# Performance work log

Measured on AMD Instinct MI355X. Metric: run time of the kernel, lower is better.

## Reference

```python
import jax, jax.numpy as jnp
import numpy as np

N, E, F_IN, DIM, HEADS, L, G, NC = 10000, 160000, 512, 256, 4, 3, 16, 10
HID = HEADS * DIM  # 1024


def gat_layer(x, src, dst, W, a_src, a_dst, b):
    # x: [N, in], W: [in, H*D], a_src/a_dst: [H, D], b: [H*D]
    h = (x @ W).reshape(N, HEADS, DIM)                       # [N,H,D]
    e_src = jnp.einsum('nhd,hd->nh', h, a_src)               # [N,H]
    e_dst = jnp.einsum('nhd,hd->nh', h, a_dst)               # [N,H]
    e = jax.nn.leaky_relu(e_src[src] + e_dst[dst], 0.2)      # [E,H]
    # segment softmax over edges grouped by destination node
    emax = jax.ops.segment_max(e, dst, num_segments=N)       # [N,H]
    ee = jnp.exp(e - emax[dst])
    denom = jax.ops.segment_sum(ee, dst, num_segments=N)     # [N,H]
    alpha = ee / denom[dst]                                  # [E,H]
    msg = h[src] * alpha[:, :, None]                         # [E,H,D]
    out = jax.ops.segment_sum(msg, dst, num_segments=N)      # [N,H,D]
    return out.reshape(N, HID) + b


def setup_inputs() -> dict:
    key = jax.random.key(0)
    ks = jax.random.split(key, 12)
    x = jax.random.normal(ks[0], (N, F_IN), dtype=jnp.float32)
    edge_index = jax.random.randint(ks[1], (2, E), 0, N, dtype=jnp.int32)
    batch = jnp.sort(jax.random.randint(ks[2], (N,), 0, G, dtype=jnp.int32))
    s0 = 1.0 / np.sqrt(F_IN)
    s1 = 1.0 / np.sqrt(HID)
    sd = 1.0 / np.sqrt(DIM)
    W0 = jax.random.normal(ks[3], (F_IN, HID), dtype=jnp.float32) * s0
    W1 = jax.random.normal(ks[4], (HID, HID), dtype=jnp.float32) * s1
    W2 = jax.random.normal(ks[5], (HID, HID), dtype=jnp.float32) * s1
    a_src = jax.random.normal(ks[6], (L, HEADS, DIM), dtype=jnp.float32) * sd
    a_dst = jax.random.normal(ks[7], (L, HEADS, DIM), dtype=jnp.float32) * sd
    bias = jnp.zeros((L, HID), dtype=jnp.float32)
    fc_w = jax.random.normal(ks[8], (HID, NC), dtype=jnp.float32) * s1
    fc_b = jnp.zeros((NC,), dtype=jnp.float32)
    return {"x": x, "edge_index": edge_index, "batch": batch, "W0": W0,
            "W1": W1, "W2": W2, "a_src": a_src, "a_dst": a_dst,
            "bias": bias, "fc_w": fc_w, "fc_b": fc_b}


def reference(x, edge_index, batch, W0, W1, W2, a_src, a_dst, bias, fc_w, fc_b):
    # add self-loops (PyG GATConv default)
    loop = jnp.arange(N, dtype=edge_index.dtype)
    src = jnp.concatenate([edge_index[0], loop])
    dst = jnp.concatenate([edge_index[1], loop])
    Ws = [W0, W1, W2]
    h = x
    for l in range(L):
        h = gat_layer(h, src, dst, Ws[l], a_src[l], a_dst[l], bias[l])
        h = jax.nn.relu(h)  # Dropout(0.5) is identity in eval mode
    # global mean pool over graphs
    sums = jax.ops.segment_sum(h, batch, num_segments=G)            # [G,HID]
    cnts = jax.ops.segment_sum(jnp.ones((N,), h.dtype), batch, num_segments=G)
    pooled = sums / jnp.maximum(cnts, 1.0)[:, None]
    logits = pooled @ fc_w + fc_b
    return jax.nn.log_softmax(logits, axis=-1)
```

## Files before the change

kernel.cpp:

```cpp
#include <hip/hip_runtime.h>
#include <math.h>

#define NNODES 10000
#define HID    1024
#define NHEADS 4
#define NGRAPH 16
#define NCLS   10

typedef __attribute__((ext_vector_type(8))) short bf16x8;
typedef __attribute__((ext_vector_type(8))) ushort u16x8;
typedef __attribute__((ext_vector_type(4))) float f32x4;
typedef __attribute__((ext_vector_type(2))) float f32x2;

__device__ __forceinline__ ushort bf16r(float f) {
    union { float f; unsigned u; } x; x.f = f;
    unsigned r = x.u + 0x7FFFu + ((x.u >> 16) & 1u);
    return (ushort)(r >> 16);
}
__device__ __forceinline__ float bf16f(ushort u) {
    union { unsigned u; float f; } x; x.u = ((unsigned)u) << 16;
    return x.f;
}
__device__ __forceinline__ float leaky(float e) { return e > 0.f ? e : 0.2f * e; }


__global__ void k_hist(const int* __restrict__ dstArr, int* __restrict__ counts,
                       const int* __restrict__ batch, int* __restrict__ gstart,
                       int* __restrict__ gend, int E, int N) {
    int e = blockIdx.x * 256 + threadIdx.x;
    int total = E + N;
    if (e < total) {
        int d = (e < E) ? dstArr[e] : (e - E);
        atomicAdd(&counts[d], 1);
    }
    if (e < N) {
        int g = batch[e];
        if (e == 0 || batch[e - 1] != g) gstart[g] = e;
        if (e == N - 1 || batch[e + 1] != g) gend[g] = e + 1;
    }
}

__global__ __launch_bounds__(1024) void k_scan(const int* __restrict__ counts,
                                               int* __restrict__ row_ptr, int N) {
    __shared__ int lds[1024];
    int t = threadIdx.x;
    const int C = (N + 1023) / 1024;
    int base = t * C;
    int s = 0;
    for (int i = 0; i < C; ++i)
        if (base + i < N) s += counts[base + i];
    lds[t] = s;
    __syncthreads();
    for (int off = 1; off < 1024; off <<= 1) {
        int add = (t >= off) ? lds[t - off] : 0;
        __syncthreads();
        lds[t] += add;
        __syncthreads();
    }
    int run = lds[t] - s;
    for (int i = 0; i < C; ++i) {
        if (base + i < N) {
            row_ptr[base + i] = run;
            run += counts[base + i];
        }
    }
    if (t == 1023) row_ptr[N] = lds[1023];
}

__global__ void k_scatter(const int* __restrict__ srcArr, const int* __restrict__ dstArr,
                          const int* __restrict__ row_ptr, int* __restrict__ fill,
                          int* __restrict__ col, int E) {
    int e = blockIdx.x * 256 + threadIdx.x;
    int total = E + NNODES;
    if (e < total) {
        int s, d;
        if (e < E) { s = srcArr[e]; d = dstArr[e]; }
        else       { s = d = e - E; }
        int pos = row_ptr[d] + atomicAdd(&fill[d], 1);
        col[pos] = s;
    }
}


__global__ void k_f32_to_bf16(const float* __restrict__ in, ushort* __restrict__ out, int n4) {
    int i = blockIdx.x * 256 + threadIdx.x;
    if (i < n4) {
        float4 v = ((const float4*)in)[i];
        ushort4 o;
        o.x = bf16r(v.x); o.y = bf16r(v.y); o.z = bf16r(v.z); o.w = bf16r(v.w);
        ((ushort4*)out)[i] = o;
    }
}

__global__ __launch_bounds__(256) void k_wT3(const float* __restrict__ W0,
                                             const float* __restrict__ W1,
                                             const float* __restrict__ W2,
                                             ushort* __restrict__ w0t,
                                             ushort* __restrict__ w1t,
                                             ushort* __restrict__ w2t) {
    __shared__ ushort tile[32][33];
    int z = blockIdx.z;
    const float* W = (z == 0) ? W0 : (z == 1) ? W1 : W2;
    ushort* Wt     = (z == 0) ? w0t : (z == 1) ? w1t : w2t;
    int K          = (z == 0) ? 512 : HID;
    int bx = blockIdx.x;
    int by = blockIdx.y;
    if (by * 32 >= K) return;
    int tx = threadIdx.x & 31, ty = threadIdx.x >> 5;
#pragma unroll
    for (int i = 0; i < 32; i += 8) {
        int k  = by * 32 + ty + i;
        int nn = bx * 32 + tx;
        tile[ty + i][tx] = bf16r(W[(size_t)k * HID + nn]);
    }
    __syncthreads();
#pragma unroll
    for (int i = 0; i < 32; i += 8) {
        int nn = bx * 32 + ty + i;
        int k  = by * 32 + tx;
        Wt[(size_t)nn * K + k] = tile[tx][ty + i];
    }
}


#define BM 128
#define BN 128
#define BK 64

__global__ __launch_bounds__(256) void k_gemm_bf16(const ushort* __restrict__ A,
                                                   const ushort* __restrict__ Bt,
                                                   ushort* __restrict__ C, int M, int K) {
    __shared__ ushort As[BM * BK];
    __shared__ ushort Bs[BN * BK];
    const int t    = threadIdx.x;
    const int lane = t & 63;
    const int w    = t >> 6;
    const int wr   = w >> 1, wc = w & 1;
    const int bm   = blockIdx.y * BM;
    const int bn   = blockIdx.x * BN;

    f32x4 acc[4][4] = {};

    const int r_  = t >> 3;
    const int cp_ = t & 7;

    const ushort* aSrc[4];
    const ushort* bSrc[4];
#pragma unroll
    for (int i = 0; i < 4; ++i) {
        int r  = i * 32 + r_;
        int c  = cp_ ^ (r & 7);
        int ga = bm + r; if (ga >= M) ga = M - 1;
        aSrc[i] = &A[(size_t)ga * K + c * 8];
        bSrc[i] = &Bt[(size_t)(bn + r) * K + c * 8];
    }

    for (int k0 = 0; k0 < K; k0 += BK) {
        __syncthreads();
#pragma unroll
        for (int i = 0; i < 4; ++i) {
            int fc = i * 256 + t;
            __builtin_amdgcn_global_load_lds(
                (const __attribute__((address_space(1))) unsigned*)(aSrc[i] + k0),
                (__attribute__((address_space(3))) unsigned*)&As[fc * 8], 16, 0, 0);
            __builtin_amdgcn_global_load_lds(
                (const __attribute__((address_space(1))) unsigned*)(bSrc[i] + k0),
                (__attribute__((address_space(3))) unsigned*)&Bs[fc * 8], 16, 0, 0);
        }
        __syncthreads();

#pragma unroll
        for (int s = 0; s < 2; ++s) {
            const int kc = s * 4 + (lane >> 4);
            bf16x8 a[4], b[4];
#pragma unroll
            for (int m = 0; m < 4; ++m) {
                int row = wr * 64 + m * 16 + (lane & 15);
                int ch  = kc ^ (row & 7);
                a[m] = *(const bf16x8*)&As[row * BK + ch * 8];
            }
#pragma unroll
            for (int n = 0; n < 4; ++n) {
                int cl = wc * 64 + n * 16 + (lane & 15);
                int ch = kc ^ (cl & 7);
                b[n] = *(const bf16x8*)&Bs[cl * BK + ch * 8];
            }
#pragma unroll
            for (int m = 0; m < 4; ++m)
#pragma unroll
                for (int n = 0; n < 4; ++n)
                    acc[m][n] = __builtin_amdgcn_mfma_f32_16x16x32_bf16(a[m], b[n], acc[m][n], 0, 0, 0);
        }
    }

#pragma unroll
    for (int m = 0; m < 4; ++m) {
        int row0 = bm + wr * 64 + m * 16 + (lane >> 4) * 4;
#pragma unroll
        for (int n = 0; n < 4; ++n) {
            int coln = bn + wc * 64 + n * 16 + (lane & 15);
#pragma unroll
            for (int j = 0; j < 4; ++j) {
                int row = row0 + j;
                if (row < M) C[(size_t)row * HID + coln] = bf16r(acc[m][n][j]);
            }
        }
    }
}


__global__ __launch_bounds__(256) void k_edotv(const ushort* __restrict__ proj,
                                               const float* __restrict__ asrc,
                                               const float* __restrict__ adst,
                                               float* __restrict__ esrc,
                                               float* __restrict__ edst,
                                               unsigned char* __restrict__ proj8) {
    int lane = threadIdx.x & 63;
    int n = blockIdx.x * 4 + (threadIdx.x >> 6);
    int h = lane >> 4;
    int c0 = lane * 16;
    u16x8 p0 = *(const u16x8*)&proj[(size_t)n * HID + c0];
    u16x8 p1 = *(const u16x8*)&proj[(size_t)n * HID + c0 + 8];
    float f[16];
#pragma unroll
    for (int i = 0; i < 8; ++i) {
        f[i]     = bf16f((ushort)p0[i]);
        f[8 + i] = bf16f((ushort)p1[i]);
    }
    float ds_ = 0.f, dd = 0.f;
#pragma unroll
    for (int i = 0; i < 16; ++i) {
        ds_ += f[i] * asrc[c0 + i];
        dd  += f[i] * adst[c0 + i];
    }
    unsigned wv[4];
#pragma unroll
    for (int q = 0; q < 4; ++q) {
        int v = 0;
        v = __builtin_amdgcn_cvt_pk_fp8_f32(f[q * 4 + 0], f[q * 4 + 1], v, false);
        v = __builtin_amdgcn_cvt_pk_fp8_f32(f[q * 4 + 2], f[q * 4 + 3], v, true);
        wv[q] = (unsigned)v;
    }
    *(uint4*)(proj8 + (size_t)n * HID + c0) = make_uint4(wv[0], wv[1], wv[2], wv[3]);

#pragma unroll
    for (int off = 8; off > 0; off >>= 1) {
        ds_ += __shfl_xor(ds_, off);
        dd  += __shfl_xor(dd, off);
    }
    if ((lane & 15) == 0) {
        esrc[n * NHEADS + h] = ds_;
        edst[n * NHEADS + h] = dd;
    }
}


__global__ __launch_bounds__(256) void k_agg(const unsigned char* __restrict__ proj8,
                                             const float* __restrict__ esrc,
                                             const float* __restrict__ edst,
                                             const int* __restrict__ row_ptr,
                                             const int* __restrict__ col,
                                             const float* __restrict__ bias,
                                             ushort* __restrict__ hb16) {
    __shared__ float aLds[4][64][NHEADS];

    const int nb   = threadIdx.x >> 6;
    const int nid  = blockIdx.x * 4 + nb;
    const int lane = threadIdx.x & 63;
    const int h    = lane >> 4;
    const int beg  = row_ptr[nid], end = row_ptr[nid + 1];
    const int deg  = end - beg;
    const bool fast = (deg <= 64);

    const float4 ed = *(const float4*)&edst[nid * 4];
    float mh, invh;

    if (fast) {
        float e0[4];
        const bool has = lane < deg;
        float m0 = -1e30f, m1 = -1e30f, m2 = -1e30f, m3 = -1e30f;
        if (has) {
            float4 es = *(const float4*)&esrc[col[beg + lane] * 4];
            e0[0] = leaky(es.x + ed.x); e0[1] = leaky(es.y + ed.y);
            e0[2] = leaky(es.z + ed.z); e0[3] = leaky(es.w + ed.w);
            m0 = e0[0]; m1 = e0[1]; m2 = e0[2]; m3 = e0[3];
        }
#pragma unroll
        for (int off = 32; off > 0; off >>= 1) {
            m0 = fmaxf(m0, __shfl_xor(m0, off)); m1 = fmaxf(m1, __shfl_xor(m1, off));
            m2 = fmaxf(m2, __shfl_xor(m2, off)); m3 = fmaxf(m3, __shfl_xor(m3, off));
        }
        float d0 = 0.f, d1 = 0.f, d2 = 0.f, d3 = 0.f;
        if (has) {
            e0[0] = __expf(e0[0] - m0); d0 = e0[0];
            e0[1] = __expf(e0[1] - m1); d1 = e0[1];
            e0[2] = __expf(e0[2] - m2); d2 = e0[2];
            e0[3] = __expf(e0[3] - m3); d3 = e0[3];
        }
#pragma unroll
        for (int off = 32; off > 0; off >>= 1) {
            d0 += __shfl_xor(d0, off); d1 += __shfl_xor(d1, off);
            d2 += __shfl_xor(d2, off); d3 += __shfl_xor(d3, off);
        }
        if (has) {
            float4 a4 = make_float4(e0[0] / d0, e0[1] / d1, e0[2] / d2, e0[3] / d3);
            *(float4*)&aLds[nb][lane][0] = a4;
        }
    } else {
        float m0 = -1e30f, m1 = -1e30f, m2 = -1e30f, m3 = -1e30f;
        for (int j = beg + lane; j < end; j += 64) {
            float4 es = *(const float4*)&esrc[col[j] * 4];
            m0 = fmaxf(m0, leaky(es.x + ed.x)); m1 = fmaxf(m1, leaky(es.y + ed.y));
            m2 = fmaxf(m2, leaky(es.z + ed.z)); m3 = fmaxf(m3, leaky(es.w + ed.w));
        }
#pragma unroll
        for (int off = 32; off > 0; off >>= 1) {
            m0 = fmaxf(m0, __shfl_xor(m0, off)); m1 = fmaxf(m1, __shfl_xor(m1, off));
            m2 = fmaxf(m2, __shfl_xor(m2, off)); m3 = fmaxf(m3, __shfl_xor(m3, off));
        }
        float d0 = 0.f, d1 = 0.f, d2 = 0.f, d3 = 0.f;
        for (int j = beg + lane; j < end; j += 64) {
            float4 es = *(const float4*)&esrc[col[j] * 4];
            d0 += __expf(leaky(es.x + ed.x) - m0); d1 += __expf(leaky(es.y + ed.y) - m1);
            d2 += __expf(leaky(es.z + ed.z) - m2); d3 += __expf(leaky(es.w + ed.w) - m3);
        }
#pragma unroll
        for (int off = 32; off > 0; off >>= 1) {
            d0 += __shfl_xor(d0, off); d1 += __shfl_xor(d1, off);
            d2 += __shfl_xor(d2, off); d3 += __shfl_xor(d3, off);
        }
        mh   = (h == 0) ? m0 : (h == 1) ? m1 : (h == 2) ? m2 : m3;
        invh = 1.f / ((h == 0) ? d0 : (h == 1) ? d1 : (h == 2) ? d2 : d3);
    }

    const unsigned char* pbase = proj8 + lane * 16;
    float acc[16] = {};

#define FMA1(A, V)                                                           \
    {                                                                        \
        f32x2 q01_ = __builtin_amdgcn_cvt_pk_f32_fp8(V.x, false);            \
        f32x2 q23_ = __builtin_amdgcn_cvt_pk_f32_fp8(V.x, true);             \
        f32x2 q45_ = __builtin_amdgcn_cvt_pk_f32_fp8(V.y, false);            \
        f32x2 q67_ = __builtin_amdgcn_cvt_pk_f32_fp8(V.y, true);             \
        f32x2 q89_ = __builtin_amdgcn_cvt_pk_f32_fp8(V.z, false);            \
        f32x2 qAB_ = __builtin_amdgcn_cvt_pk_f32_fp8(V.z, true);             \
        f32x2 qCD_ = __builtin_amdgcn_cvt_pk_f32_fp8(V.w, false);            \
        f32x2 qEF_ = __builtin_amdgcn_cvt_pk_f32_fp8(V.w, true);             \
        acc[0]  += A * q01_[0]; acc[1]  += A * q01_[1];                      \
        acc[2]  += A * q23_[0]; acc[3]  += A * q23_[1];                      \
        acc[4]  += A * q45_[0]; acc[5]  += A * q45_[1];                      \
        acc[6]  += A * q67_[0]; acc[7]  += A * q67_[1];                      \
        acc[8]  += A * q89_[0]; acc[9]  += A * q89_[1];                      \
        acc[10] += A * qAB_[0]; acc[11] += A * qAB_[1];                      \
        acc[12] += A * qCD_[0]; acc[13] += A * qCD_[1];                      \
        acc[14] += A * qEF_[0]; acc[15] += A * qEF_[1];                      \
    }

    if (fast) {
#define LOADCHUNK(cb, A0, A1, A2, A3, V0, V1, V2, V3)                        \
    {                                                                        \
        int4 cc_ = *(const int4*)&col[cb];                                   \
        bool m0_ = ((cb) + 0 >= beg) & ((cb) + 0 < end);                     \
        bool m1_ = ((cb) + 1 >= beg) & ((cb) + 1 < end);                     \
        bool m2_ = ((cb) + 2 >= beg) & ((cb) + 2 < end);                     \
        bool m3_ = ((cb) + 3 >= beg) & ((cb) + 3 < end);                     \
        int s0_ = m0_ ? cc_.x : 0; int s1_ = m1_ ? cc_.y : 0;                \
        int s2_ = m2_ ? cc_.z : 0; int s3_ = m3_ ? cc_.w : 0;                \
        int l0_ = m0_ ? (cb) + 0 - beg : 0; int l1_ = m1_ ? (cb) + 1 - beg : 0; \
        int l2_ = m2_ ? (cb) + 2 - beg : 0; int l3_ = m3_ ? (cb) + 3 - beg : 0; \
        A0 = m0_ ? aLds[nb][l0_][h] : 0.f;                                   \
        A1 = m1_ ? aLds[nb][l1_][h] : 0.f;                                   \
        A2 = m2_ ? aLds[nb][l2_][h] : 0.f;                                   \
        A3 = m3_ ? aLds[nb][l3_][h] : 0.f;                                   \
        V0 = *(const uint4*)(pbase + (size_t)s0_ * HID);                     \
        V1 = *(const uint4*)(pbase + (size_t)s1_ * HID);                     \
        V2 = *(const uint4*)(pbase + (size_t)s2_ * HID);                     \
        V3 = *(const uint4*)(pbase + (size_t)s3_ * HID);                     \
    }
#define FMACHUNK(A0, A1, A2, A3, V0, V1, V2, V3)                             \
    { FMA1(A0, V0) FMA1(A1, V1) FMA1(A2, V2) FMA1(A3, V3) }

        int c = beg & ~3;
        float a0, a1, a2, a3;
        uint4 v0, v1, v2, v3;
        LOADCHUNK(c, a0, a1, a2, a3, v0, v1, v2, v3);
        for (c += 4; c < end; c += 4) {
            float na0, na1, na2, na3;
            uint4 nv0, nv1, nv2, nv3;
            LOADCHUNK(c, na0, na1, na2, na3, nv0, nv1, nv2, nv3);
            FMACHUNK(a0, a1, a2, a3, v0, v1, v2, v3);
            a0 = na0; a1 = na1; a2 = na2; a3 = na3;
            v0 = nv0; v1 = nv1; v2 = nv2; v3 = nv3;
        }
        FMACHUNK(a0, a1, a2, a3, v0, v1, v2, v3);
#undef LOADCHUNK
#undef FMACHUNK
    } else {
        const float edn = (h == 0) ? ed.x : (h == 1) ? ed.y : (h == 2) ? ed.z : ed.w;
        for (int j = beg; j < end; ++j) {
            int s = col[j];
            float e = leaky(esrc[s * 4 + h] + edn);
            float a = __expf(e - mh) * invh;
            uint4 v = *(const uint4*)(pbase + (size_t)s * HID);
            FMA1(a, v);
        }
    }
#undef FMA1

    u16x8 o0, o1;
#pragma unroll
    for (int i = 0; i < 8; ++i) {
        o0[i] = bf16r(fmaxf(acc[i]     + bias[lane * 16 + i],     0.f));
        o1[i] = bf16r(fmaxf(acc[8 + i] + bias[lane * 16 + 8 + i], 0.f));
    }
    *(u16x8*)&hb16[(size_t)nid * HID + lane * 16]     = o0;
    *(u16x8*)&hb16[(size_t)nid * HID + lane * 16 + 8] = o1;
}


#define PCHUNK 32
__global__ __launch_bounds__(256) void k_pool(const ushort* __restrict__ h,
                                              const int* __restrict__ batch,
                                              float* __restrict__ pooled, int N) {
    int c  = blockIdx.y * 256 + threadIdx.x;
    int n0 = blockIdx.x * PCHUNK;
    int n1 = n0 + PCHUNK; if (n1 > N) n1 = N;
    int g = batch[n0];
    float acc = 0.f;
    for (int n = n0; n < n1; ++n) {
        int gn = batch[n];
        if (gn != g) {
            atomicAdd(&pooled[g * HID + c], acc);
            acc = 0.f; g = gn;
        }
        acc += bf16f(h[(size_t)n * HID + c]);
    }
    atomicAdd(&pooled[g * HID + c], acc);
}

__global__ __launch_bounds__(256) void k_fc(const float* __restrict__ pooled,
                                            const int* __restrict__ gstart,
                                            const int* __restrict__ gend,
                                            const float* __restrict__ fcw,
                                            const float* __restrict__ fcb,
                                            float* __restrict__ out) {
    int g = blockIdx.x;
    int t = threadIdx.x;
    float invc = 1.f / fmaxf((float)(gend[g] - gstart[g]), 1.f);
    __shared__ float red[NCLS][256];
    float part[NCLS];
#pragma unroll
    for (int c = 0; c < NCLS; ++c) part[c] = 0.f;
    for (int k = t; k < HID; k += 256) {
        float v = pooled[g * HID + k] * invc;
#pragma unroll
        for (int c = 0; c < NCLS; ++c) part[c] += v * fcw[k * NCLS + c];
    }
#pragma unroll
    for (int c = 0; c < NCLS; ++c) red[c][t] = part[c];
    __syncthreads();
    for (int off = 128; off > 0; off >>= 1) {
        if (t < off) {
#pragma unroll
            for (int c = 0; c < NCLS; ++c) red[c][t] += red[c][t + off];
        }
        __syncthreads();
    }
    if (t == 0) {
        float logits[NCLS];
        float mx = -1e30f;
#pragma unroll
        for (int c = 0; c < NCLS; ++c) {
            logits[c] = red[c][0] + fcb[c];
            mx = fmaxf(mx, logits[c]);
        }
        float se = 0.f;
#pragma unroll
        for (int c = 0; c < NCLS; ++c) se += expf(logits[c] - mx);
        float lse = mx + logf(se);
#pragma unroll
        for (int c = 0; c < NCLS; ++c) out[g * NCLS + c] = logits[c] - lse;
    }
}


extern "C" void kernel_launch(void* const* d_in, const int* in_sizes, int n_in,
                              void* d_out, int out_size, void* d_ws, size_t ws_size,
                              hipStream_t stream) {
    const float* x    = (const float*)d_in[0];
    const int*   ei   = (const int*)d_in[1];
    const int*   batch= (const int*)d_in[2];
    const float* W0   = (const float*)d_in[3];
    const float* W1   = (const float*)d_in[4];
    const float* W2   = (const float*)d_in[5];
    const float* asrc = (const float*)d_in[6];
    const float* adst = (const float*)d_in[7];
    const float* bias = (const float*)d_in[8];
    const float* fcw  = (const float*)d_in[9];
    const float* fcb  = (const float*)d_in[10];
    float* out = (float*)d_out;

    const int E = in_sizes[1] / 2;
    const int N = NNODES;
    const int NE = E + N;

    char* ws = (char*)d_ws;
    size_t off = 0;
    auto alloc = [&](size_t bytes) { void* p = ws + off; off += (bytes + 255) & ~(size_t)255; return p; };
    ushort* projb  = (ushort*)alloc((size_t)N * HID * 2);
    unsigned char* proj8 = (unsigned char*)alloc((size_t)N * HID);
    ushort* hb16   = (ushort*)alloc((size_t)N * HID * 2);
    ushort* xb16   = (ushort*)alloc((size_t)N * 512 * 2);
    ushort* w0t    = (ushort*)alloc((size_t)HID * 512 * 2);
    ushort* w1t    = (ushort*)alloc((size_t)HID * HID * 2);
    ushort* w2t    = (ushort*)alloc((size_t)HID * HID * 2);
    float*  esrc   = (float*)alloc((size_t)N * NHEADS * 4);
    float*  edst   = (float*)alloc((size_t)N * NHEADS * 4);
    int*    row_ptr= (int*)alloc((size_t)(N + 1) * 4);
    int*    col    = (int*)alloc((size_t)(NE + 16) * 4);
    size_t zstart = off;
    int*    counts  = (int*)alloc((size_t)N * 4);
    int*    fill    = (int*)alloc((size_t)N * 4);
    int*    gstart  = (int*)alloc(NGRAPH * 4);
    int*    gend    = (int*)alloc(NGRAPH * 4);
    float*  pooled  = (float*)alloc(NGRAPH * HID * 4);
    size_t zbytes = off - zstart;
    (void)ws_size;

    const int* srcArr = ei;
    const int* dstArr = ei + E;

    hipMemsetAsync(ws + zstart, 0, zbytes, stream);
    hipMemsetAsync(col + NE, 0, 16 * 4, stream);

    int nbE = (NE + 255) / 256;
    k_hist<<<nbE, 256, 0, stream>>>(dstArr, counts, batch, gstart, gend, E, N);
    k_scan<<<1, 1024, 0, stream>>>(counts, row_ptr, N);
    k_scatter<<<nbE, 256, 0, stream>>>(srcArr, dstArr, row_ptr, fill, col, E);

    k_f32_to_bf16<<<(N * 512 / 4 + 255) / 256, 256, 0, stream>>>(x, xb16, N * 512 / 4);
    k_wT3<<<dim3(32, HID / 32, 3), 256, 0, stream>>>(W0, W1, W2, w0t, w1t, w2t);

    dim3 gemmGrid(HID / BN, (N + BM - 1) / BM);

    k_gemm_bf16<<<gemmGrid, 256, 0, stream>>>(xb16, w0t, projb, N, 512);
    k_edotv<<<N / 4, 256, 0, stream>>>(projb, asrc + 0 * HID, adst + 0 * HID, esrc, edst, proj8);
    k_agg<<<N / 4, 256, 0, stream>>>(proj8, esrc, edst, row_ptr, col, bias + 0 * HID, hb16);

    k_gemm_bf16<<<gemmGrid, 256, 0, stream>>>(hb16, w1t, projb, N, HID);
    k_edotv<<<N / 4, 256, 0, stream>>>(projb, asrc + 1 * HID, adst + 1 * HID, esrc, edst, proj8);
    k_agg<<<N / 4, 256, 0, stream>>>(proj8, esrc, edst, row_ptr, col, bias + 1 * HID, hb16);

    k_gemm_bf16<<<gemmGrid, 256, 0, stream>>>(hb16, w2t, projb, N, HID);
    k_edotv<<<N / 4, 256, 0, stream>>>(projb, asrc + 2 * HID, adst + 2 * HID, esrc, edst, proj8);
    k_agg<<<N / 4, 256, 0, stream>>>(proj8, esrc, edst, row_ptr, col, bias + 2 * HID, hb16);

    dim3 poolGrid((N + PCHUNK - 1) / PCHUNK, HID / 256);
    k_pool<<<poolGrid, 256, 0, stream>>>(hb16, batch, pooled, N);
    k_fc<<<NGRAPH, 256, 0, stream>>>(pooled, gstart, gend, fcw, fcb, out);
}
```

Baseline: 266.1 us.

## Fuse attention dot products and fp8 quantization into GEMM epilogue

The GEMM epilogue now computes per-64-column partial attention scores (e_src, e_dst) and writes fp8 projections directly, eliminating the separate k_edotv kernel and the bf16 projection buffer round-trip. Partial sums are stored as 16 slots per node, and the aggregation kernel sums 4 partials per head when reading. This removes a full read/write pass over the N×1024 projection, at the cost of byte-granular scattered fp8 stores in the epilogue and 4x larger gathered score reads in aggregation.

```diff
diff --git a/kernel.cpp b/kernel.cpp
--- a/kernel.cpp
+++ b/kernel.cpp
@@ -129,7 +129,12 @@
 
 __global__ __launch_bounds__(256) void k_gemm_bf16(const ushort* __restrict__ A,
                                                    const ushort* __restrict__ Bt,
-                                                   ushort* __restrict__ C, int M, int K) {
+                                                   unsigned char* __restrict__ proj8,
+                                                   int M, int K,
+                                                   const float* __restrict__ asrcL,
+                                                   const float* __restrict__ adstL,
+                                                   float* __restrict__ esrcP,
+                                                   float* __restrict__ edstP) {
     __shared__ ushort As[BM * BK];
     __shared__ ushort Bs[BN * BK];
     const int t    = threadIdx.x;
@@ -193,71 +198,50 @@
         }
     }
 
+    const int hcol0 = bn + wc * 64;
+    const int slot  = hcol0 >> 6;
+    float as_[4], ad_[4];
+#pragma unroll
+    for (int n = 0; n < 4; ++n) {
+        int coln = hcol0 + n * 16 + (lane & 15);
+        as_[n] = asrcL[coln];
+        ad_[n] = adstL[coln];
+    }
 #pragma unroll
     for (int m = 0; m < 4; ++m) {
         int row0 = bm + wr * 64 + m * 16 + (lane >> 4) * 4;
 #pragma unroll
-        for (int n = 0; n < 4; ++n) {
-            int coln = bn + wc * 64 + n * 16 + (lane & 15);
-#pragma unroll
-            for (int j = 0; j < 4; ++j) {
-                int row = row0 + j;
-                if (row < M) C[(size_t)row * HID + coln] = bf16r(acc[m][n][j]);
+        for (int j = 0; j < 4; ++j) {
+            int row = row0 + j;
+            float ps = 0.f, pd = 0.f;
+#pragma unroll
+            for (int n = 0; n < 4; ++n) {
+                float v = acc[m][n][j];
+                ps += v * as_[n];
+                pd += v * ad_[n];
+                if (row < M) {
+                    int r8 = __builtin_amdgcn_cvt_pk_fp8_f32(v, v, 0, false);
+                    proj8[(size_t)row * HID + hcol0 + n * 16 + (lane & 15)] =
+                        (unsigned char)(r8 & 0xFF);
+                }
             }
-        }
-    }
-}
-
-
-__global__ __launch_bounds__(256) void k_edotv(const ushort* __restrict__ proj,
-                                               const float* __restrict__ asrc,
-                                               const float* __restrict__ adst,
-                                               float* __restrict__ esrc,
-                                               float* __restrict__ edst,
-                                               unsigned char* __restrict__ proj8) {
-    int lane = threadIdx.x & 63;
-    int n = blockIdx.x * 4 + (threadIdx.x >> 6);
-    int h = lane >> 4;
-    int c0 = lane * 16;
-    u16x8 p0 = *(const u16x8*)&proj[(size_t)n * HID + c0];
-    u16x8 p1 = *(const u16x8*)&proj[(size_t)n * HID + c0 + 8];
-    float f[16];
-#pragma unroll
-    for (int i = 0; i < 8; ++i) {
-        f[i]     = bf16f((ushort)p0[i]);
-        f[8 + i] = bf16f((ushort)p1[i]);
-    }
-    float ds_ = 0.f, dd = 0.f;
-#pragma unroll
-    for (int i = 0; i < 16; ++i) {
-        ds_ += f[i] * asrc[c0 + i];
-        dd  += f[i] * adst[c0 + i];
-    }
-    unsigned wv[4];
-#pragma unroll
-    for (int q = 0; q < 4; ++q) {
-        int v = 0;
-        v = __builtin_amdgcn_cvt_pk_fp8_f32(f[q * 4 + 0], f[q * 4 + 1], v, false);
-        v = __builtin_amdgcn_cvt_pk_fp8_f32(f[q * 4 + 2], f[q * 4 + 3], v, true);
-        wv[q] = (unsigned)v;
-    }
-    *(uint4*)(proj8 + (size_t)n * HID + c0) = make_uint4(wv[0], wv[1], wv[2], wv[3]);
-
-#pragma unroll
-    for (int off = 8; off > 0; off >>= 1) {
-        ds_ += __shfl_xor(ds_, off);
-        dd  += __shfl_xor(dd, off);
-    }
-    if ((lane & 15) == 0) {
-        esrc[n * NHEADS + h] = ds_;
-        edst[n * NHEADS + h] = dd;
+#pragma unroll
+            for (int off = 1; off < 16; off <<= 1) {
+                ps += __shfl_xor(ps, off);
+                pd += __shfl_xor(pd, off);
+            }
+            if ((lane & 15) == 0 && row < M) {
+                esrcP[row * 16 + slot] = ps;
+                edstP[row * 16 + slot] = pd;
+            }
+        }
     }
 }
 
 
 __global__ __launch_bounds__(256) void k_agg(const unsigned char* __restrict__ proj8,
-                                             const float* __restrict__ esrc,
-                                             const float* __restrict__ edst,
+                                             const float* __restrict__ esrcP,
+                                             const float* __restrict__ edstP,
                                              const int* __restrict__ row_ptr,
                                              const int* __restrict__ col,
                                              const float* __restrict__ bias,
@@ -272,7 +256,12 @@
     const int deg  = end - beg;
     const bool fast = (deg <= 64);
 
-    const float4 ed = *(const float4*)&edst[nid * 4];
+    const float4* edP = (const float4*)&edstP[(size_t)nid * 16];
+    float4 eda = edP[0], edb = edP[1], edc = edP[2], edd = edP[3];
+    const float ed0 = eda.x + eda.y + eda.z + eda.w;
+    const float ed1 = edb.x + edb.y + edb.z + edb.w;
+    const float ed2 = edc.x + edc.y + edc.z + edc.w;
+    const float ed3 = edd.x + edd.y + edd.z + edd.w;
     float mh, invh;
 
     if (fast) {
@@ -280,9 +269,12 @@
         const bool has = lane < deg;
         float m0 = -1e30f, m1 = -1e30f, m2 = -1e30f, m3 = -1e30f;
         if (has) {
-            float4 es = *(const float4*)&esrc[col[beg + lane] * 4];
-            e0[0] = leaky(es.x + ed.x); e0[1] = leaky(es.y + ed.y);
-            e0[2] = leaky(es.z + ed.z); e0[3] = leaky(es.w + ed.w);
+            const float4* eP = (const float4*)&esrcP[(size_t)col[beg + lane] * 16];
+            float4 sa = eP[0], sb = eP[1], sc = eP[2], sd = eP[3];
+            e0[0] = leaky(sa.x + sa.y + sa.z + sa.w + ed0);
+            e0[1] = leaky(sb.x + sb.y + sb.z + sb.w + ed1);
+            e0[2] = leaky(sc.x + sc.y + sc.z + sc.w + ed2);
+            e0[3] = leaky(sd.x + sd.y + sd.z + sd.w + ed3);
             m0 = e0[0]; m1 = e0[1]; m2 = e0[2]; m3 = e0[3];
         }
 #pragma unroll
@@ -309,9 +301,12 @@
     } else {
         float m0 = -1e30f, m1 = -1e30f, m2 = -1e30f, m3 = -1e30f;
         for (int j = beg + lane; j < end; j += 64) {
-            float4 es = *(const float4*)&esrc[col[j] * 4];
-            m0 = fmaxf(m0, leaky(es.x + ed.x)); m1 = fmaxf(m1, leaky(es.y + ed.y));
-            m2 = fmaxf(m2, leaky(es.z + ed.z)); m3 = fmaxf(m3, leaky(es.w + ed.w));
+            const float4* eP = (const float4*)&esrcP[(size_t)col[j] * 16];
+            float4 sa = eP[0], sb = eP[1], sc = eP[2], sd = eP[3];
+            m0 = fmaxf(m0, leaky(sa.x + sa.y + sa.z + sa.w + ed0));
+            m1 = fmaxf(m1, leaky(sb.x + sb.y + sb.z + sb.w + ed1));
+            m2 = fmaxf(m2, leaky(sc.x + sc.y + sc.z + sc.w + ed2));
+            m3 = fmaxf(m3, leaky(sd.x + sd.y + sd.z + sd.w + ed3));
         }
 #pragma unroll
         for (int off = 32; off > 0; off >>= 1) {
@@ -320,9 +315,12 @@
         }
         float d0 = 0.f, d1 = 0.f, d2 = 0.f, d3 = 0.f;
         for (int j = beg + lane; j < end; j += 64) {
-            float4 es = *(const float4*)&esrc[col[j] * 4];
-            d0 += __expf(leaky(es.x + ed.x) - m0); d1 += __expf(leaky(es.y + ed.y) - m1);
-            d2 += __expf(leaky(es.z + ed.z) - m2); d3 += __expf(leaky(es.w + ed.w) - m3);
+            const float4* eP = (const float4*)&esrcP[(size_t)col[j] * 16];
+            float4 sa = eP[0], sb = eP[1], sc = eP[2], sd = eP[3];
+            d0 += __expf(leaky(sa.x + sa.y + sa.z + sa.w + ed0) - m0);
+            d1 += __expf(leaky(sb.x + sb.y + sb.z + sb.w + ed1) - m1);
+            d2 += __expf(leaky(sc.x + sc.y + sc.z + sc.w + ed2) - m2);
+            d3 += __expf(leaky(sd.x + sd.y + sd.z + sd.w + ed3) - m3);
         }
 #pragma unroll
         for (int off = 32; off > 0; off >>= 1) {
@@ -396,10 +394,12 @@
 #undef LOADCHUNK
 #undef FMACHUNK
     } else {
-        const float edn = (h == 0) ? ed.x : (h == 1) ? ed.y : (h == 2) ? ed.z : ed.w;
+        const float edn = (h == 0) ? ed0 : (h == 1) ? ed1 : (h == 2) ? ed2 : ed3;
         for (int j = beg; j < end; ++j) {
             int s = col[j];
-            float e = leaky(esrc[s * 4 + h] + edn);
+            float es = esrcP[(size_t)s * 16 + 4 * h]     + esrcP[(size_t)s * 16 + 4 * h + 1]
+                     + esrcP[(size_t)s * 16 + 4 * h + 2] + esrcP[(size_t)s * 16 + 4 * h + 3];
+            float e = leaky(es + edn);
             float a = __expf(e - mh) * invh;
             uint4 v = *(const uint4*)(pbase + (size_t)s * HID);
             FMA1(a, v);
@@ -507,15 +507,14 @@
     char* ws = (char*)d_ws;
     size_t off = 0;
     auto alloc = [&](size_t bytes) { void* p = ws + off; off += (bytes + 255) & ~(size_t)255; return p; };
-    ushort* projb  = (ushort*)alloc((size_t)N * HID * 2);
     unsigned char* proj8 = (unsigned char*)alloc((size_t)N * HID);
     ushort* hb16   = (ushort*)alloc((size_t)N * HID * 2);
     ushort* xb16   = (ushort*)alloc((size_t)N * 512 * 2);
     ushort* w0t    = (ushort*)alloc((size_t)HID * 512 * 2);
     ushort* w1t    = (ushort*)alloc((size_t)HID * HID * 2);
     ushort* w2t    = (ushort*)alloc((size_t)HID * HID * 2);
-    float*  esrc   = (float*)alloc((size_t)N * NHEADS * 4);
-    float*  edst   = (float*)alloc((size_t)N * NHEADS * 4);
+    float*  esrcP  = (float*)alloc((size_t)N * 16 * 4);
+    float*  edstP  = (float*)alloc((size_t)N * 16 * 4);
     int*    row_ptr= (int*)alloc((size_t)(N + 1) * 4);
     int*    col    = (int*)alloc((size_t)(NE + 16) * 4);
     size_t zstart = off;
@@ -543,17 +542,17 @@
 
     dim3 gemmGrid(HID / BN, (N + BM - 1) / BM);
 
-    k_gemm_bf16<<<gemmGrid, 256, 0, stream>>>(xb16, w0t, projb, N, 512);
-    k_edotv<<<N / 4, 256, 0, stream>>>(projb, asrc + 0 * HID, adst + 0 * HID, esrc, edst, proj8);
-    k_agg<<<N / 4, 256, 0, stream>>>(proj8, esrc, edst, row_ptr, col, bias + 0 * HID, hb16);
-
-    k_gemm_bf16<<<gemmGrid, 256, 0, stream>>>(hb16, w1t, projb, N, HID);
-    k_edotv<<<N / 4, 256, 0, stream>>>(projb, asrc + 1 * HID, adst + 1 * HID, esrc, edst, proj8);
-    k_agg<<<N / 4, 256, 0, stream>>>(proj8, esrc, edst, row_ptr, col, bias + 1 * HID, hb16);
-
-    k_gemm_bf16<<<gemmGrid, 256, 0, stream>>>(hb16, w2t, projb, N, HID);
-    k_edotv<<<N / 4, 256, 0, stream>>>(projb, asrc + 2 * HID, adst + 2 * HID, esrc, edst, proj8);
-    k_agg<<<N / 4, 256, 0, stream>>>(proj8, esrc, edst, row_ptr, col, bias + 2 * HID, hb16);
+    k_gemm_bf16<<<gemmGrid, 256, 0, stream>>>(xb16, w0t, proj8, N, 512,
+                                              asrc + 0 * HID, adst + 0 * HID, esrcP, edstP);
+    k_agg<<<N / 4, 256, 0, stream>>>(proj8, esrcP, edstP, row_ptr, col, bias + 0 * HID, hb16);
+
+    k_gemm_bf16<<<gemmGrid, 256, 0, stream>>>(hb16, w1t, proj8, N, HID,
+                                              asrc + 1 * HID, adst + 1 * HID, esrcP, edstP);
+    k_agg<<<N / 4, 256, 0, stream>>>(proj8, esrcP, edstP, row_ptr, col, bias + 1 * HID, hb16);
+
+    k_gemm_bf16<<<gemmGrid, 256, 0, stream>>>(hb16, w2t, proj8, N, HID,
+                                              asrc + 2 * HID, adst + 2 * HID, esrcP, edstP);
+    k_agg<<<N / 4, 256, 0, stream>>>(proj8, esrcP, edstP, row_ptr, col, bias + 2 * HID, hb16);
 
     dim3 poolGrid((N + PCHUNK - 1) / PCHUNK, HID / 256);
     k_pool<<<poolGrid, 256, 0, stream>>>(hb16, batch, pooled, N);
```

After: 254.3 us. 1.05x faster.
